# Optimization experiments

Measured on AMD Instinct MI355X. Metric: run time of the kernel, lower is better.

Reference implementation:

```python
import jax, jax.numpy as jnp
import numpy as np

EMBED_DIM = 1024
NUM_HEADS = 16
HEAD_DIM = EMBED_DIM // NUM_HEADS
B, N = 4, 2048


def setup_inputs() -> dict:
    key = jax.random.key(0)
    ks = jax.random.split(key, 9)
    s = 1.0 / np.sqrt(EMBED_DIM)  # mimic sensible init scale
    return {
        "q": jax.random.normal(ks[0], (B, N, EMBED_DIM), dtype=jnp.float32),
        "Wq": jax.random.normal(ks[1], (EMBED_DIM, EMBED_DIM), dtype=jnp.float32) * s,
        "bq": jnp.zeros((EMBED_DIM,), dtype=jnp.float32),
        "Wk": jax.random.normal(ks[2], (EMBED_DIM, EMBED_DIM), dtype=jnp.float32) * s,
        "bk": jnp.zeros((EMBED_DIM,), dtype=jnp.float32),
        "Wv": jax.random.normal(ks[3], (EMBED_DIM, EMBED_DIM), dtype=jnp.float32) * s,
        "bv": jnp.zeros((EMBED_DIM,), dtype=jnp.float32),
        "Wo": jax.random.normal(ks[4], (EMBED_DIM, EMBED_DIM), dtype=jnp.float32) * s,
        "bo": jnp.zeros((EMBED_DIM,), dtype=jnp.float32),
    }


def _split_heads(x):
    # [B, N, C] -> [B, H, N, Dh]
    b, n, _ = x.shape
    return x.reshape(b, n, NUM_HEADS, HEAD_DIM).transpose(0, 2, 1, 3)


def reference(q, Wq, bq, Wk, bk, Wv, bv, Wo, bo):
    b, n, c = q.shape
    # self-attention: k = v = q input; nn.Linear computes x @ W.T + b
    qh = _split_heads(q @ Wq.T + bq)
    kh = _split_heads(q @ Wk.T + bk)
    vh = _split_heads(q @ Wv.T + bv)
    # [B, H, N, N]
    attn_logits = jnp.einsum("bhqd,bhkd->bhqk", qh, kh) / np.sqrt(HEAD_DIM).astype(np.float32)
    attn_scores = jax.nn.softmax(attn_logits, axis=-1)
    # dropout rate 0.0 / eval mode -> identity
    attn_w = jnp.einsum("bhqk,bhkd->bhqd", attn_scores, vh)
    attn_w = attn_w.transpose(0, 2, 1, 3).reshape(b, n, c)  # [B, N, C]
    output = attn_w @ Wo.T + bo
    return (output, attn_w)
```

## Files before the change

### kernel.cpp

```cpp
#include <hip/hip_runtime.h>

typedef float  f32x4  __attribute__((ext_vector_type(4)));
typedef float  f32x16 __attribute__((ext_vector_type(16)));
typedef __bf16 bf16x2 __attribute__((ext_vector_type(2)));
typedef __bf16 bf16x4 __attribute__((ext_vector_type(4)));
typedef __bf16 bf16x8 __attribute__((ext_vector_type(8)));
typedef unsigned int u32;
typedef u32 u32x4 __attribute__((ext_vector_type(4)));

#define MFMA16(a, b, c) __builtin_amdgcn_mfma_f32_16x16x32_bf16((a), (b), (c), 0, 0, 0)
#define MFMA32(a, b, c) __builtin_amdgcn_mfma_f32_32x32x16_bf16((a), (b), (c), 0, 0, 0)

constexpr int EMB  = 1024;
constexpr int NSEQ = 2048;
constexpr int NB   = 4;
constexpr int NH   = 16;
constexpr int DH   = 64;
constexpr size_t HSTRIDE = (size_t)NSEQ * DH;
constexpr size_t MAT     = (size_t)NB * NSEQ * EMB;
constexpr size_t WSZ     = (size_t)EMB * EMB;
constexpr int    BSEQ    = NB * NSEQ;
constexpr float  QSCALE  = 0.18033688011112042f;

__device__ __forceinline__ __bf16 f2bf(float f) { return (__bf16)f; }

__device__ __forceinline__ u32 pkbf(float a, float b) {
  bf16x2 t = {(__bf16)a, (__bf16)b};
  return __builtin_bit_cast(u32, t);
}

__device__ __forceinline__ int swz(int a) { return a ^ (((a >> 7) & 7) << 4); }

__device__ __forceinline__ void gll16(const void* g, void* l) {
  __builtin_amdgcn_global_load_lds((const __attribute__((address_space(1))) unsigned*)g,
                                   (__attribute__((address_space(3))) unsigned*)l, 16, 0, 0);
}

__global__ __launch_bounds__(256) void cvt_all(const float* __restrict__ x,
                                               const float* __restrict__ w0,
                                               const float* __restrict__ w1,
                                               const float* __restrict__ w2,
                                               const float* __restrict__ w3,
                                               __bf16* __restrict__ Xbf,
                                               __bf16* __restrict__ Wbf) {
  const int xblocks = (int)(MAT / 4 / 256);
  const int wslice  = (int)(WSZ / 4 / 256);
  const float* src;
  __bf16* dst;
  size_t idx;
  if (blockIdx.x < (unsigned)xblocks) {
    src = x; dst = Xbf;
    idx = (size_t)blockIdx.x * 256 + threadIdx.x;
  } else {
    int j = blockIdx.x - xblocks;
    int z = j / wslice, r = j % wslice;
    const float* srcs[4] = {w0, w1, w2, w3};
    src = srcs[z];
    dst = Wbf + (size_t)z * WSZ;
    idx = (size_t)r * 256 + threadIdx.x;
  }
  f32x4 v = *reinterpret_cast<const f32x4*>(src + idx * 4);
  bf16x4 o = {f2bf(v[0]), f2bf(v[1]), f2bf(v[2]), f2bf(v[3])};
  *reinterpret_cast<bf16x4*>(dst + idx * 4) = o;
}

__global__ __launch_bounds__(256) void qkv3(const __bf16* __restrict__ Xbf,
                                            const __bf16* __restrict__ Wbf,
                                            const float* __restrict__ bq,
                                            const float* __restrict__ bk,
                                            const float* __restrict__ bv,
                                            __bf16* __restrict__ Qw,
                                            __bf16* __restrict__ Kw,
                                            __bf16* __restrict__ Vtw) {
  __shared__ __align__(16) __bf16 sA[128 * 64];
  __shared__ __align__(16) __bf16 sW[3][64 * 64];
  const int t = threadIdx.x;
  const int lane = t & 63, w = t >> 6;
  const int l15 = lane & 15, g = lane >> 4;

  int flat = blockIdx.x + 16 * blockIdx.y;
  int logical = (flat & 7) * 128 + (flat >> 3);
  const int m0 = (logical >> 4) * 128, n0 = (logical & 15) * 64;

  const char* Ac  = (const char*)Xbf;
  const char* Wc[3] = {(const char*)(Wbf + 0 * WSZ),
                       (const char*)(Wbf + 1 * WSZ),
                       (const char*)(Wbf + 2 * WSZ)};

  const int srow = lane >> 3;
  const int scol = ((lane & 7) ^ srow) * 16;

  int offA[2][2], offB[4][2];
#pragma unroll
  for (int i = 0; i < 2; ++i)
#pragma unroll
    for (int ks = 0; ks < 2; ++ks) {
      int ra = w * 32 + i * 16 + l15;
      offA[i][ks] = (ra * 128 + ((ks * 64 + g * 16) ^ ((l15 & 7) << 4))) >> 1;
    }
#pragma unroll
  for (int i = 0; i < 4; ++i)
#pragma unroll
    for (int ks = 0; ks < 2; ++ks) {
      int rb = i * 16 + l15;
      offB[i][ks] = (rb * 128 + ((ks * 64 + g * 16) ^ ((l15 & 7) << 4))) >> 1;
    }

  f32x4 acc[3][2][4];
#pragma unroll
  for (int m = 0; m < 3; ++m)
#pragma unroll
    for (int i = 0; i < 2; ++i)
#pragma unroll
      for (int j = 0; j < 4; ++j) acc[m][i][j] = f32x4{0.f, 0.f, 0.f, 0.f};

#pragma unroll 1
  for (int k0 = 0; k0 < EMB; k0 += 64) {
#pragma unroll
    for (int p = 0; p < 4; ++p) {
      int c = p * 4 + w;
      gll16(Ac + (size_t)(m0 + c * 8 + srow) * (EMB * 2) + k0 * 2 + scol, sA + c * 512);
    }
#pragma unroll
    for (int p = 0; p < 2; ++p) {
      int c = p * 4 + w;
      size_t rowB = (size_t)(n0 + c * 8 + srow) * (EMB * 2) + k0 * 2 + scol;
#pragma unroll
      for (int mat = 0; mat < 3; ++mat)
        gll16(Wc[mat] + rowB, &sW[mat][c * 512]);
    }
    __syncthreads();
#pragma unroll
    for (int ks = 0; ks < 2; ++ks) {
      bf16x8 af[2];
#pragma unroll
      for (int i = 0; i < 2; ++i)
        af[i] = *reinterpret_cast<const bf16x8*>(&sA[offA[i][ks]]);
#pragma unroll
      for (int mat = 0; mat < 3; ++mat) {
        bf16x8 bf[4];
#pragma unroll
        for (int i = 0; i < 4; ++i)
          bf[i] = *reinterpret_cast<const bf16x8*>(&sW[mat][offB[i][ks]]);
#pragma unroll
        for (int mi = 0; mi < 2; ++mi)
#pragma unroll
          for (int ni = 0; ni < 4; ++ni)
            acc[mat][mi][ni] = MFMA16(af[mi], bf[ni], acc[mat][mi][ni]);
      }
    }
    __syncthreads();
  }

  const int hh = n0 >> 6;
#pragma unroll
  for (int mi = 0; mi < 2; ++mi)
#pragma unroll
    for (int ni = 0; ni < 4; ++ni) {
      int cg = n0 + ni * 16 + l15;
      int d = cg & (DH - 1);
#pragma unroll
      for (int j = 0; j < 4; ++j) {
        int rg = m0 + w * 32 + mi * 16 + g * 4 + j;
        int bb = rg >> 11, r = rg & (NSEQ - 1);
        size_t hb = (size_t)(bb * NH + hh);
        size_t idx = (hb * NSEQ + r) * DH + d;
        Qw[idx] = f2bf((acc[0][mi][ni][j] + bq[cg]) * QSCALE);
        Kw[idx] = f2bf(acc[1][mi][ni][j] + bk[cg]);
      }
      float bvc = bv[cg];
      int rg0 = m0 + w * 32 + mi * 16 + g * 4;
      bf16x4 pv = {f2bf(acc[2][mi][ni][0] + bvc), f2bf(acc[2][mi][ni][1] + bvc),
                   f2bf(acc[2][mi][ni][2] + bvc), f2bf(acc[2][mi][ni][3] + bvc)};
      *reinterpret_cast<bf16x4*>(Vtw + (size_t)cg * BSEQ + rg0) = pv;
    }
}

__device__ __forceinline__ void gemm_loop(__bf16* sA, __bf16* sB,
                                          const __bf16* __restrict__ A,
                                          const __bf16* __restrict__ W,
                                          int m0, int n0, f32x4 (&acc)[4][4]) {
  const int t = threadIdx.x;
  const int lane = t & 63, w = t >> 6;
  const int wr = w >> 1, wc = w & 1;
  const int l15 = lane & 15, g = lane >> 4;
  const char* Ac = (const char*)A;
  const char* Wc = (const char*)W;
  const int srow = lane >> 3;
  const int scol = ((lane & 7) ^ srow) * 16;

  int offA[4][2], offB[4][2];
#pragma unroll
  for (int i = 0; i < 4; ++i)
#pragma unroll
    for (int ks = 0; ks < 2; ++ks) {
      int ra = wr * 64 + i * 16 + l15;
      int rb = wc * 64 + i * 16 + l15;
      offA[i][ks] = (ra * 128 + ((ks * 64 + g * 16) ^ ((l15 & 7) << 4))) >> 1;
      offB[i][ks] = (rb * 128 + ((ks * 64 + g * 16) ^ ((l15 & 7) << 4))) >> 1;
    }

#pragma unroll 1
  for (int k0 = 0; k0 < EMB; k0 += 64) {
#pragma unroll
    for (int p = 0; p < 4; ++p) {
      int c = p * 4 + w;
      gll16(Ac + (size_t)(m0 + c * 8 + srow) * (EMB * 2) + k0 * 2 + scol, sA + c * 512);
      gll16(Wc + (size_t)(n0 + c * 8 + srow) * (EMB * 2) + k0 * 2 + scol, sB + c * 512);
    }
    __syncthreads();
    bf16x8 af[4][2], bfr[4][2];
#pragma unroll
    for (int i = 0; i < 4; ++i)
#pragma unroll
      for (int ks = 0; ks < 2; ++ks) {
        af[i][ks]  = *reinterpret_cast<const bf16x8*>(sA + offA[i][ks]);
        bfr[i][ks] = *reinterpret_cast<const bf16x8*>(sB + offB[i][ks]);
      }
#pragma unroll
    for (int ks = 0; ks < 2; ++ks)
#pragma unroll
      for (int mi = 0; mi < 4; ++mi)
#pragma unroll
        for (int ni = 0; ni < 4; ++ni)
          acc[mi][ni] = MFMA16(af[mi][ks], bfr[ni][ks], acc[mi][ni]);
    __syncthreads();
  }
}

__global__ __launch_bounds__(256) void oproj_bf(const __bf16* __restrict__ Abf,
                                                const __bf16* __restrict__ W,
                                                const float* __restrict__ bias,
                                                float* __restrict__ outp) {
  __shared__ __align__(16) __bf16 smem[2][128 * 64];
  int flat = blockIdx.x + 8 * blockIdx.y;
  int logical = (flat & 7) * 64 + (flat >> 3);
  const int m0 = (logical >> 3) * 128, n0 = (logical & 7) * 128;

  f32x4 acc[4][4];
#pragma unroll
  for (int i = 0; i < 4; ++i)
#pragma unroll
    for (int j = 0; j < 4; ++j) acc[i][j] = f32x4{0.f, 0.f, 0.f, 0.f};

  gemm_loop(smem[0], smem[1], Abf, W, m0, n0, acc);

  const int lane = threadIdx.x & 63, w = threadIdx.x >> 6;
  const int wr = w >> 1, wc = w & 1, l15 = lane & 15, g = lane >> 4;
#pragma unroll
  for (int mi = 0; mi < 4; ++mi)
#pragma unroll
    for (int ni = 0; ni < 4; ++ni)
#pragma unroll
      for (int j = 0; j < 4; ++j) {
        int rg = m0 + wr * 64 + mi * 16 + g * 4 + j;
        int cg = n0 + wc * 64 + ni * 16 + l15;
        outp[(size_t)rg * EMB + cg] = acc[mi][ni][j] + bias[cg];
      }
}

__global__ __launch_bounds__(512) void flash_kernel(const __bf16* __restrict__ Qb,
                                                    const __bf16* __restrict__ Kb,
                                                    const __bf16* __restrict__ Vtb,
                                                    float* __restrict__ attnw,
                                                    __bf16* __restrict__ attnw_bf) {
  __shared__ __align__(16) __bf16 lds[2][16384];
  const int t = threadIdx.x;
  const int lane = t & 63, w = t >> 6;
  const int l31 = lane & 31, hi = lane >> 5;

  int flat = blockIdx.x + 8 * (blockIdx.y + NH * blockIdx.z);
  int logical = (flat & 7) * 64 + (flat >> 3);
  const int qt = logical & 7, h = (logical >> 3) & 15, b = logical >> 7;

  const size_t hoff = ((size_t)(b * NH + h)) * HSTRIDE;
  const __bf16* Qh = Qb + hoff;
  const char* Kc = (const char*)(Kb + hoff);
  const char* Vc = (const char*)(Vtb + (size_t)(h * DH) * BSEQ + (size_t)b * NSEQ);
  const int q0 = qt * 256 + w * 32;

  bf16x8 qf[4];
#pragma unroll
  for (int ds = 0; ds < 4; ++ds)
    qf[ds] = *reinterpret_cast<const bf16x8*>(Qh + (size_t)(q0 + l31) * DH + ds * 16 + hi * 8);

  int koff[2][4], voff[4][2];
#pragma unroll
  for (int kt32 = 0; kt32 < 2; ++kt32)
#pragma unroll
    for (int ds = 0; ds < 4; ++ds)
      koff[kt32][ds] = swz((kt32 * 32 + l31) * 128 + ds * 32 + hi * 16) >> 1;
#pragma unroll
  for (int c = 0; c < 4; ++c)
#pragma unroll
    for (int db = 0; db < 2; ++db)
      voff[c][db] = swz((db * 32 + l31) * 128 + c * 32 + hi * 16) >> 1;

  auto stage = [&](int bf, int kt) {
#pragma unroll
    for (int hh = 0; hh < 2; ++hh) {
      int L = w * 1024 + lane * 16;
      int s = swz(L);
      gll16(Kc + (size_t)(kt + hh * 64) * 128 + s, &lds[bf][hh * 4096 + w * 512]);
      int d = s >> 7, rem = s & 127;
      gll16(Vc + (size_t)d * (BSEQ * 2) + (kt + hh * 64) * 2 + rem,
            &lds[bf][8192 + hh * 4096 + w * 512]);
    }
  };

  f32x16 o0{}, o1{};
  float lsum = 0.f;
  const f32x16 kZero{};

  stage(0, 0);
  __syncthreads();

#pragma unroll 1
  for (int it = 0; it < NSEQ / 128; ++it) {
    const int cur = it & 1;
    if (it + 1 < NSEQ / 128) stage(cur ^ 1, (it + 1) * 128);

#pragma unroll
    for (int sub = 0; sub < 2; ++sub) {
      const __bf16* Kl = lds[cur] + sub * 4096;
      const __bf16* Vl = lds[cur] + 8192 + sub * 4096;

      bf16x8 kf[2][4];
#pragma unroll
      for (int kt32 = 0; kt32 < 2; ++kt32)
#pragma unroll
        for (int ds = 0; ds < 4; ++ds)
          kf[kt32][ds] = *reinterpret_cast<const bf16x8*>(Kl + koff[kt32][ds]);

      f32x16 s0, s1;
      __builtin_amdgcn_s_setprio(1);
      s0 = MFMA32(kf[0][0], qf[0], kZero);
      s1 = MFMA32(kf[1][0], qf[0], kZero);
#pragma unroll
      for (int ds = 1; ds < 4; ++ds) s0 = MFMA32(kf[0][ds], qf[ds], s0);
#pragma unroll
      for (int ds = 1; ds < 4; ++ds) s1 = MFMA32(kf[1][ds], qf[ds], s1);
      __builtin_amdgcn_s_setprio(0);

      bf16x8 vf[4][2];
#pragma unroll
      for (int c = 0; c < 4; ++c)
#pragma unroll
        for (int db = 0; db < 2; ++db)
          vf[c][db] = *reinterpret_cast<const bf16x8*>(Vl + voff[c][db]);

#pragma unroll
      for (int r = 0; r < 16; ++r) s0[r] = __builtin_amdgcn_exp2f(s0[r]);
#pragma unroll
      for (int r = 0; r < 16; ++r) s1[r] = __builtin_amdgcn_exp2f(s1[r]);

      {
        float t0 = ((s0[0] + s0[1]) + (s0[2] + s0[3])) + ((s0[4] + s0[5]) + (s0[6] + s0[7]));
        float t1 = ((s0[8] + s0[9]) + (s0[10] + s0[11])) + ((s0[12] + s0[13]) + (s0[14] + s0[15]));
        float t2 = ((s1[0] + s1[1]) + (s1[2] + s1[3])) + ((s1[4] + s1[5]) + (s1[6] + s1[7]));
        float t3 = ((s1[8] + s1[9]) + (s1[10] + s1[11])) + ((s1[12] + s1[13]) + (s1[14] + s1[15]));
        lsum += (t0 + t1) + (t2 + t3);
      }

      u32 pk0[8], pk1[8];
#pragma unroll
      for (int j = 0; j < 8; ++j) pk0[j] = pkbf(s0[2 * j], s0[2 * j + 1]);
#pragma unroll
      for (int j = 0; j < 8; ++j) pk1[j] = pkbf(s1[2 * j], s1[2 * j + 1]);

      auto pv_step = [&](u32& a0, u32& a1, u32& a2, u32& a3, int c) {
        asm("v_permlane32_swap_b32 %0, %1" : "+v"(a0), "+v"(a2));
        asm("v_permlane32_swap_b32 %0, %1" : "+v"(a1), "+v"(a3));
        u32x4 wv = {a0, a1, a2, a3};
        bf16x8 pa = __builtin_bit_cast(bf16x8, wv);
        o0 = MFMA32(pa, vf[c][0], o0);
        o1 = MFMA32(pa, vf[c][1], o1);
      };
      __builtin_amdgcn_s_setprio(1);
      pv_step(pk0[0], pk0[1], pk0[2], pk0[3], 0);
      pv_step(pk0[4], pk0[5], pk0[6], pk0[7], 1);
      pv_step(pk1[0], pk1[1], pk1[2], pk1[3], 2);
      pv_step(pk1[4], pk1[5], pk1[6], pk1[7], 3);
      __builtin_amdgcn_s_setprio(0);
    }

    __syncthreads();
  }

  lsum += __shfl_xor(lsum, 32);
  float inv = 1.0f / lsum;

#pragma unroll
  for (int r = 0; r < 16; ++r) {
    int qq = (r & 3) + 8 * (r >> 2) + 4 * hi;
    float invq = __shfl(inv, qq);
    int row = q0 + qq;
    float v0 = o0[r] * invq, v1 = o1[r] * invq;
    float* base = attnw + ((size_t)(b * NSEQ + row)) * EMB + h * DH;
    base[l31]      = v0;
    base[32 + l31] = v1;
    __bf16* bb2 = attnw_bf + ((size_t)(b * NSEQ + row)) * EMB + h * DH;
    bb2[l31]      = f2bf(v0);
    bb2[32 + l31] = f2bf(v1);
  }
}

extern "C" void kernel_launch(void* const* d_in, const int* in_sizes, int n_in,
                              void* d_out, int out_size, void* d_ws, size_t ws_size,
                              hipStream_t stream) {
  const float* q  = (const float*)d_in[0];
  const float* Wq = (const float*)d_in[1];
  const float* bq = (const float*)d_in[2];
  const float* Wk = (const float*)d_in[3];
  const float* bk = (const float*)d_in[4];
  const float* Wv = (const float*)d_in[5];
  const float* bv = (const float*)d_in[6];
  const float* Wo = (const float*)d_in[7];
  const float* bo = (const float*)d_in[8];

  float* outp  = (float*)d_out;
  float* attnw = outp + MAT;

  __bf16* Qw   = (__bf16*)d_ws;
  __bf16* Kw   = Qw + MAT;
  __bf16* Vtw  = Qw + 2 * MAT;
  __bf16* Xbf  = Qw + 3 * MAT;
  __bf16* Wbf  = Qw + 4 * MAT;

  const int xblocks = (int)(MAT / 4 / 256);
  const int wblocks = (int)(4 * WSZ / 4 / 256);
  cvt_all<<<xblocks + wblocks, 256, 0, stream>>>(q, Wq, Wk, Wv, Wo, Xbf, Wbf);

  qkv3<<<dim3(16, 64), 256, 0, stream>>>(Xbf, Wbf, bq, bk, bv, Qw, Kw, Vtw);

  flash_kernel<<<dim3(8, NH, NB), 512, 0, stream>>>(Qw, Kw, Vtw, attnw, Xbf);

  oproj_bf<<<dim3(8, 64), 256, 0, stream>>>(Xbf, Wbf + 3 * WSZ, bo, outp);
}
```

Measured before the change: 184.7 us.

## Pre-tile K and V in MFMA fragment order so flash loads are contiguous

The QKV projection now writes K and V straight into a per-head, per-64-row tiled layout that matches the MFMA fragment order used by the attention kernel. The flash kernel then stages each tile with fully contiguous 16-byte global-to-LDS copies and reads fragments at simple lane-linear offsets, with no swizzle arithmetic. This removes the strided V-transpose gather and the swizzled address math. The cost is scattered, less coalesced stores in the QKV epilogue, and LDS reads that may now hit bank conflicts.

```diff
diff --git a/kernel.cpp b/kernel.cpp
--- a/kernel.cpp
+++ b/kernel.cpp
@@ -19,7 +19,6 @@
 constexpr size_t HSTRIDE = (size_t)NSEQ * DH;
 constexpr size_t MAT     = (size_t)NB * NSEQ * EMB;
 constexpr size_t WSZ     = (size_t)EMB * EMB;
-constexpr int    BSEQ    = NB * NSEQ;
 constexpr float  QSCALE  = 0.18033688011112042f;
 
 __device__ __forceinline__ __bf16 f2bf(float f) { return (__bf16)f; }
@@ -71,7 +70,7 @@
                                             const float* __restrict__ bv,
                                             __bf16* __restrict__ Qw,
                                             __bf16* __restrict__ Kw,
-                                            __bf16* __restrict__ Vtw) {
+                                            __bf16* __restrict__ Vw) {
   __shared__ __align__(16) __bf16 sA[128 * 64];
   __shared__ __align__(16) __bf16 sW[3][64 * 64];
   const int t = threadIdx.x;
@@ -164,15 +163,22 @@
         int rg = m0 + w * 32 + mi * 16 + g * 4 + j;
         int bb = rg >> 11, r = rg & (NSEQ - 1);
         size_t hb = (size_t)(bb * NH + hh);
-        size_t idx = (hb * NSEQ + r) * DH + d;
-        Qw[idx] = f2bf((acc[0][mi][ni][j] + bq[cg]) * QSCALE);
-        Kw[idx] = f2bf(acc[1][mi][ni][j] + bk[cg]);
+        Qw[(hb * NSEQ + r) * DH + d] = f2bf((acc[0][mi][ni][j] + bq[cg]) * QSCALE);
+        size_t kidx = hb * HSTRIDE + (size_t)(r >> 6) * 4096
+                    + (size_t)(((((r >> 5) & 1) << 2) + (d >> 4)) * 512)
+                    + (size_t)(((((d >> 3) & 1) << 5) + (r & 31)) * 8) + (d & 7);
+        Kw[kidx] = f2bf(acc[1][mi][ni][j] + bk[cg]);
       }
       float bvc = bv[cg];
       int rg0 = m0 + w * 32 + mi * 16 + g * 4;
+      int bb = rg0 >> 11, kv0 = rg0 & (NSEQ - 1);
+      int kvL = kv0 & 63;
+      size_t vaddr = (size_t)(bb * NH + hh) * HSTRIDE + (size_t)(kv0 >> 6) * 4096
+                   + (size_t)(((((kvL >> 4) & 3) << 1) + (d >> 5)) * 512)
+                   + (size_t)(((((kvL >> 3) & 1) << 5) + (d & 31)) * 8) + (kvL & 7);
       bf16x4 pv = {f2bf(acc[2][mi][ni][0] + bvc), f2bf(acc[2][mi][ni][1] + bvc),
                    f2bf(acc[2][mi][ni][2] + bvc), f2bf(acc[2][mi][ni][3] + bvc)};
-      *reinterpret_cast<bf16x4*>(Vtw + (size_t)cg * BSEQ + rg0) = pv;
+      *reinterpret_cast<bf16x4*>(Vw + vaddr) = pv;
     }
 }
 
@@ -261,7 +267,7 @@
 
 __global__ __launch_bounds__(512) void flash_kernel(const __bf16* __restrict__ Qb,
                                                     const __bf16* __restrict__ Kb,
-                                                    const __bf16* __restrict__ Vtb,
+                                                    const __bf16* __restrict__ Vb,
                                                     float* __restrict__ attnw,
                                                     __bf16* __restrict__ attnw_bf) {
   __shared__ __align__(16) __bf16 lds[2][16384];
@@ -276,7 +282,7 @@
   const size_t hoff = ((size_t)(b * NH + h)) * HSTRIDE;
   const __bf16* Qh = Qb + hoff;
   const char* Kc = (const char*)(Kb + hoff);
-  const char* Vc = (const char*)(Vtb + (size_t)(h * DH) * BSEQ + (size_t)b * NSEQ);
+  const char* Vc = (const char*)(Vb + hoff);
   const int q0 = qt * 256 + w * 32;
 
   bf16x8 qf[4];
@@ -284,33 +290,20 @@
   for (int ds = 0; ds < 4; ++ds)
     qf[ds] = *reinterpret_cast<const bf16x8*>(Qh + (size_t)(q0 + l31) * DH + ds * 16 + hi * 8);
 
-  int koff[2][4], voff[4][2];
-#pragma unroll
-  for (int kt32 = 0; kt32 < 2; ++kt32)
-#pragma unroll
-    for (int ds = 0; ds < 4; ++ds)
-      koff[kt32][ds] = swz((kt32 * 32 + l31) * 128 + ds * 32 + hi * 16) >> 1;
-#pragma unroll
-  for (int c = 0; c < 4; ++c)
-#pragma unroll
-    for (int db = 0; db < 2; ++db)
-      voff[c][db] = swz((db * 32 + l31) * 128 + c * 32 + hi * 16) >> 1;
-
-  auto stage = [&](int bf, int kt) {
-#pragma unroll
-    for (int hh = 0; hh < 2; ++hh) {
-      int L = w * 1024 + lane * 16;
-      int s = swz(L);
-      gll16(Kc + (size_t)(kt + hh * 64) * 128 + s, &lds[bf][hh * 4096 + w * 512]);
-      int d = s >> 7, rem = s & 127;
-      gll16(Vc + (size_t)d * (BSEQ * 2) + (kt + hh * 64) * 2 + rem,
-            &lds[bf][8192 + hh * 4096 + w * 512]);
+  auto stage = [&](int bf, int it) {
+#pragma unroll
+    for (int j = 0; j < 2; ++j) {
+      int chunk = w * 2 + j;
+      size_t src = (size_t)it * 16384 + chunk * 1024 + lane * 16;
+      gll16(Kc + src, &lds[bf][chunk * 512]);
+      gll16(Vc + src, &lds[bf][8192 + chunk * 512]);
     }
   };
 
   f32x16 o0{}, o1{};
   float lsum = 0.f;
   const f32x16 kZero{};
+  const int lofs = lane * 8;
 
   stage(0, 0);
   __syncthreads();
@@ -318,7 +311,7 @@
 #pragma unroll 1
   for (int it = 0; it < NSEQ / 128; ++it) {
     const int cur = it & 1;
-    if (it + 1 < NSEQ / 128) stage(cur ^ 1, (it + 1) * 128);
+    if (it + 1 < NSEQ / 128) stage(cur ^ 1, it + 1);
 
 #pragma unroll
     for (int sub = 0; sub < 2; ++sub) {
@@ -330,7 +323,7 @@
       for (int kt32 = 0; kt32 < 2; ++kt32)
 #pragma unroll
         for (int ds = 0; ds < 4; ++ds)
-          kf[kt32][ds] = *reinterpret_cast<const bf16x8*>(Kl + koff[kt32][ds]);
+          kf[kt32][ds] = *reinterpret_cast<const bf16x8*>(Kl + (kt32 * 4 + ds) * 512 + lofs);
 
       f32x16 s0, s1;
       __builtin_amdgcn_s_setprio(1);
@@ -347,7 +340,7 @@
       for (int c = 0; c < 4; ++c)
 #pragma unroll
         for (int db = 0; db < 2; ++db)
-          vf[c][db] = *reinterpret_cast<const bf16x8*>(Vl + voff[c][db]);
+          vf[c][db] = *reinterpret_cast<const bf16x8*>(Vl + (c * 2 + db) * 512 + lofs);
 
 #pragma unroll
       for (int r = 0; r < 16; ++r) s0[r] = __builtin_amdgcn_exp2f(s0[r]);
@@ -423,7 +416,7 @@
 
   __bf16* Qw   = (__bf16*)d_ws;
   __bf16* Kw   = Qw + MAT;
-  __bf16* Vtw  = Qw + 2 * MAT;
+  __bf16* Vw   = Qw + 2 * MAT;
   __bf16* Xbf  = Qw + 3 * MAT;
   __bf16* Wbf  = Qw + 4 * MAT;
 
@@ -431,9 +424,9 @@
   const int wblocks = (int)(4 * WSZ / 4 / 256);
   cvt_all<<<xblocks + wblocks, 256, 0, stream>>>(q, Wq, Wk, Wv, Wo, Xbf, Wbf);
 
-  qkv3<<<dim3(16, 64), 256, 0, stream>>>(Xbf, Wbf, bq, bk, bv, Qw, Kw, Vtw);
-
-  flash_kernel<<<dim3(8, NH, NB), 512, 0, stream>>>(Qw, Kw, Vtw, attnw, Xbf);
+  qkv3<<<dim3(16, 64), 256, 0, stream>>>(Xbf, Wbf, bq, bk, bv, Qw, Kw, Vw);
+
+  flash_kernel<<<dim3(8, NH, NB), 512, 0, stream>>>(Qw, Kw, Vw, attnw, Xbf);
 
   oproj_bf<<<dim3(8, 64), 256, 0, stream>>>(Xbf, Wbf + 3 * WSZ, bo, outp);
 }
```

New measurement: 185.1 us, median of 2. Within noise of the previous version (+0.3%).
